# Optimization experiments

Hardware: AMD Instinct MI355X
Metric: run time of the kernel (lower is better)

The kernel has to match this reference:

```python
import jax, jax.numpy as jnp
import numpy as np

R = 16
ALPHA = 32
SCALING = ALPHA / R  # 2.0


def setup_inputs() -> dict:
    key = jax.random.key(0)
    k_x, k_w, k_b, k_a, k_lb, k_o = jax.random.split(key, 6)
    in_f, out_f = 4096, 4096
    x = jax.random.normal(k_x, (4, 4096, in_f), dtype=jnp.float32)
    base_kernel = jax.random.normal(k_w, (in_f, out_f), dtype=jnp.float32) * 0.02
    base_bias = jax.random.normal(k_b, (out_f,), dtype=jnp.float32) * 0.02
    lora_A = jax.random.normal(k_a, (R, R), dtype=jnp.float32)
    lora_B = jax.random.normal(k_lb, (R, R), dtype=jnp.float32) * 0.02
    O = jax.random.normal(k_o, (in_f // R, out_f // R), dtype=jnp.float32)
    return {"x": x, "base_kernel": base_kernel, "base_bias": base_bias,
            "lora_A": lora_A, "lora_B": lora_B, "O": O}


def reference(x, base_kernel, base_bias, lora_A, lora_B, O) -> jnp.ndarray:
    in_f, out_f = base_kernel.shape
    # base path: x @ W + b
    base_out = jnp.dot(x, base_kernel) + base_bias
    # LoKr path: kron(A @ B, O) materialized as in the original module
    w_left = jnp.dot(lora_A, lora_B)                 # (r, r)
    lokr_update = jnp.kron(w_left, O)                # (r*in_factor, r*out_factor)
    lokr_update = lokr_update[:in_f, :out_f]
    lokr_out = jnp.dot(x, lokr_update)
    return base_out + lokr_out * SCALING
```

## Files before the change

### kernel.cpp

```cpp
#include <hip/hip_runtime.h>
#include <stdint.h>
#include <stddef.h>


#define M_TOT 16384
#define K_TOT 4096
#define N_TOT 4096
#define SCALING 2.0f
#define NT (K_TOT / 64)

typedef __attribute__((ext_vector_type(8))) short bf16x8;
typedef __attribute__((ext_vector_type(4))) float floatx4;

__device__ __forceinline__ unsigned short f32_to_bf16(float f) {
  union { float f; unsigned int u; } v; v.f = f;
  unsigned int r = 0x7fffu + ((v.u >> 16) & 1u);
  return (unsigned short)((v.u + r) >> 16);
}

__device__ __forceinline__ void async_copy16(const void* gsrc, void* ldst) {
  __builtin_amdgcn_global_load_lds(
      (const __attribute__((address_space(1))) void*)(uintptr_t)gsrc,
      (__attribute__((address_space(3))) void*)(uintptr_t)ldst,
      16, 0, 0);
}

__global__ void wleft_kernel(const float* __restrict__ A, const float* __restrict__ B,
                             float* __restrict__ wl) {
  int i = threadIdx.x >> 4, j = threadIdx.x & 15;
  float s = 0.f;
#pragma unroll
  for (int k = 0; k < 16; ++k) s += A[i * 16 + k] * B[k * 16 + j];
  wl[threadIdx.x] = s * SCALING;
}

__global__ void prep_w_kernel(const float* __restrict__ base, const float* __restrict__ O,
                              const float* __restrict__ wl, unsigned short* __restrict__ Wt) {
  __shared__ float tile[32][33];
  int n0 = blockIdx.x * 32, k0 = blockIdx.y * 32;
  int tx = threadIdx.x, ty = threadIdx.y;
#pragma unroll
  for (int r = 0; r < 32; r += 8) {
    int k = k0 + ty + r, n = n0 + tx;
    float v = base[(size_t)k * N_TOT + n]
            + wl[((k >> 8) << 4) + (n >> 8)] * O[((size_t)(k & 255) << 8) + (n & 255)];
    tile[ty + r][tx] = v;
  }
  __syncthreads();
#pragma unroll
  for (int r = 0; r < 32; r += 8) {
    int n = n0 + ty + r, k = k0 + tx;
    Wt[(size_t)n * K_TOT + k] = f32_to_bf16(tile[tx][ty + r]);
  }
}

__global__ void cvt_x_kernel(const float* __restrict__ x, unsigned short* __restrict__ xb) {
  size_t i = ((size_t)blockIdx.x * blockDim.x + threadIdx.x) * 8;
  float4 a = *(const float4*)(x + i);
  float4 b = *(const float4*)(x + i + 4);
  union { bf16x8 v; unsigned short h[8]; } u;
  u.h[0] = f32_to_bf16(a.x); u.h[1] = f32_to_bf16(a.y);
  u.h[2] = f32_to_bf16(a.z); u.h[3] = f32_to_bf16(a.w);
  u.h[4] = f32_to_bf16(b.x); u.h[5] = f32_to_bf16(b.y);
  u.h[6] = f32_to_bf16(b.z); u.h[7] = f32_to_bf16(b.w);
  *(bf16x8*)(xb + i) = u.v;
}

__global__ __launch_bounds__(512, 2) void gemm256_kernel(
    const unsigned short* __restrict__ Xb, const unsigned short* __restrict__ Wt,
    const float* __restrict__ bias, float* __restrict__ out) {
  __shared__ __align__(16) unsigned short lds[65536];

  const int tid = threadIdx.x;
  const int wave = tid >> 6, lane = tid & 63;
  const int quad = lane >> 4, lm = lane & 15;
  const int wm = wave >> 2, wn = wave & 3;

  const int wg = blockIdx.x;
  const int swz = (wg & 7) * (1024 / 8) + (wg >> 3);
  const int m0 = (swz >> 4) * 256;
  const int n0 = (swz & 15) * 256;

  const int sch = (tid & 7) ^ ((tid >> 3) & 7);
  const int rowoff = 2 * (tid >> 3) + (sch >> 2);
  const int koff = (sch & 3) * 8;
  const unsigned short* srcA = Xb + (size_t)(m0 + rowoff) * K_TOT + koff;
  const unsigned short* srcB = Wt + (size_t)(n0 + rowoff) * K_TOT + koff;

  const int pch = (((lm & 1) << 2) | quad) ^ (lm >> 1);
  const int aoff = wm * 4096 + (lm >> 1) * 64 + pch * 8;
  const int boff = wn * 2048 + (lm >> 1) * 64 + pch * 8;

  floatx4 acc[8][4];
#pragma unroll
  for (int i = 0; i < 8; ++i)
#pragma unroll
    for (int j = 0; j < 4; ++j) acc[i][j] = (floatx4){0.f, 0.f, 0.f, 0.f};

#define STAGE(tt, ss) do {                                                        \
    unsigned short* la = lds + ((((tt) & 1) * 2 + (ss)) * 8192) + tid * 8;        \
    size_t kk = (size_t)(tt) * 64 + (ss) * 32;                                    \
    async_copy16(srcA + kk, la);                                                  \
    async_copy16(srcA + kk + (size_t)128 * K_TOT, la + 4096);                     \
    async_copy16(srcB + kk, la + 32768);                                          \
    async_copy16(srcB + kk + (size_t)128 * K_TOT, la + 32768 + 4096);             \
  } while (0)

#define COMPUTE(tt, ss) do {                                                      \
    const unsigned short* Ab = lds + ((((tt) & 1) * 2 + (ss)) * 8192) + aoff;     \
    const unsigned short* Bb = lds + 32768 + ((((tt) & 1) * 2 + (ss)) * 8192) + boff; \
    bf16x8 af[8], bfr[4];                                                         \
    _Pragma("unroll") for (int i = 0; i < 8; ++i)                                 \
      af[i] = *(const bf16x8*)(Ab + i * 512);                                     \
    _Pragma("unroll") for (int j = 0; j < 4; ++j)                                 \
      bfr[j] = *(const bf16x8*)(Bb + j * 512);                                    \
    __builtin_amdgcn_s_setprio(1);                                                \
    _Pragma("unroll") for (int i = 0; i < 8; ++i)                                 \
      _Pragma("unroll") for (int j = 0; j < 4; ++j)                               \
        acc[i][j] = __builtin_amdgcn_mfma_f32_16x16x32_bf16(af[i], bfr[j], acc[i][j], 0, 0, 0); \
    __builtin_amdgcn_s_setprio(0);                                                \
  } while (0)

#define WAITBAR(n) do {                                                          \
    asm volatile("s_waitcnt vmcnt(" #n ")" ::: "memory");                        \
    __builtin_amdgcn_s_barrier();                                                \
    asm volatile("" ::: "memory");                                               \
  } while (0)

  STAGE(0, 0);
  STAGE(0, 1);
  STAGE(1, 0);
  WAITBAR(8);

  for (int t = 0; t < NT - 2; ++t) {
    STAGE(t + 1, 1);
    COMPUTE(t, 0);
    WAITBAR(8);
    STAGE(t + 2, 0);
    COMPUTE(t, 1);
    WAITBAR(8);
  }
  STAGE(NT - 1, 1);
  COMPUTE(NT - 2, 0);
  WAITBAR(8);
  COMPUTE(NT - 2, 1);
  WAITBAR(4);
  COMPUTE(NT - 1, 0);
  WAITBAR(0);
  COMPUTE(NT - 1, 1);

#undef STAGE
#undef COMPUTE
#undef WAITBAR

#pragma unroll
  for (int j = 0; j < 4; ++j) {
    int col = n0 + wn * 64 + j * 16 + lm;
    float bv = bias[col];
#pragma unroll
    for (int i = 0; i < 8; ++i) {
      int row = m0 + wm * 128 + i * 16 + quad * 4;
#pragma unroll
      for (int r = 0; r < 4; ++r)
        out[(size_t)(row + r) * N_TOT + col] = acc[i][j][r] + bv;
    }
  }
}

extern "C" void kernel_launch(void* const* d_in, const int* in_sizes, int n_in,
                              void* d_out, int out_size, void* d_ws, size_t ws_size,
                              hipStream_t stream) {
  const float* x    = (const float*)d_in[0];
  const float* base = (const float*)d_in[1];
  const float* bias = (const float*)d_in[2];
  const float* lA   = (const float*)d_in[3];
  const float* lB   = (const float*)d_in[4];
  const float* O    = (const float*)d_in[5];
  float* out = (float*)d_out;

  char* ws = (char*)d_ws;
  unsigned short* Xb = (unsigned short*)ws;
  unsigned short* Wt = (unsigned short*)(ws + (size_t)M_TOT * K_TOT * 2);
  float* wl = (float*)(ws + (size_t)M_TOT * K_TOT * 2 + (size_t)N_TOT * K_TOT * 2);

  wleft_kernel<<<1, 256, 0, stream>>>(lA, lB, wl);
  prep_w_kernel<<<dim3(N_TOT / 32, K_TOT / 32), dim3(32, 8), 0, stream>>>(base, O, wl, Wt);
  cvt_x_kernel<<<((size_t)M_TOT * K_TOT) / 8 / 256, 256, 0, stream>>>(x, Xb);
  gemm256_kernel<<<dim3(1024), 512, 0, stream>>>(Xb, Wt, bias, out);
}
```

Baseline: 959.1 us.

## Interleave GEMM main loop into half-tile phases and vectorize weight prep

The GEMM main loop now runs in four phases per K-tile. Each phase loads half the A fragments from LDS, issues a smaller async stage of A or B, then runs 16 MFMAs, so the two barriers per phase are spread through the loop. This is meant to overlap LDS reads, global-to-LDS copies and MFMA work more finely, at the cost of more barriers per tile. The weight-prep kernel switches to 64x64 tiles with float4 loads, a single hoisted Kronecker scale per block, and 16-byte bf16 stores, which cuts memory transactions.

Measured after the change: 961.9 us. About the same (+0.3%).

```diff
diff --git a/kernel.cpp b/kernel.cpp
--- a/kernel.cpp
+++ b/kernel.cpp
@@ -11,6 +11,7 @@
 
 typedef __attribute__((ext_vector_type(8))) short bf16x8;
 typedef __attribute__((ext_vector_type(4))) float floatx4;
+typedef __attribute__((ext_vector_type(4))) unsigned int uint4v;
 
 __device__ __forceinline__ unsigned short f32_to_bf16(float f) {
   union { float f; unsigned int u; } v; v.f = f;
@@ -36,21 +37,31 @@
 
 __global__ void prep_w_kernel(const float* __restrict__ base, const float* __restrict__ O,
                               const float* __restrict__ wl, unsigned short* __restrict__ Wt) {
-  __shared__ float tile[32][33];
-  int n0 = blockIdx.x * 32, k0 = blockIdx.y * 32;
-  int tx = threadIdx.x, ty = threadIdx.y;
-#pragma unroll
-  for (int r = 0; r < 32; r += 8) {
-    int k = k0 + ty + r, n = n0 + tx;
-    float v = base[(size_t)k * N_TOT + n]
-            + wl[((k >> 8) << 4) + (n >> 8)] * O[((size_t)(k & 255) << 8) + (n & 255)];
-    tile[ty + r][tx] = v;
+  __shared__ float tile[64][65];
+  const int tid = threadIdx.x;
+  const int n0 = blockIdx.x * 64, k0 = blockIdx.y * 64;
+  const float wlv = wl[((k0 >> 8) << 4) + (n0 >> 8)];
+  const float* Obase = O + ((size_t)(k0 & 255) << 8) + (n0 & 255);
+#pragma unroll
+  for (int rep = 0; rep < 4; ++rep) {
+    int idx = rep * 256 + tid;
+    int row = idx >> 4, c4 = (idx & 15) * 4;
+    float4 b4 = *(const float4*)(base + (size_t)(k0 + row) * N_TOT + n0 + c4);
+    float4 o4 = *(const float4*)(Obase + (size_t)row * 256 + c4);
+    tile[row][c4 + 0] = b4.x + wlv * o4.x;
+    tile[row][c4 + 1] = b4.y + wlv * o4.y;
+    tile[row][c4 + 2] = b4.z + wlv * o4.z;
+    tile[row][c4 + 3] = b4.w + wlv * o4.w;
   }
   __syncthreads();
 #pragma unroll
-  for (int r = 0; r < 32; r += 8) {
-    int n = n0 + ty + r, k = k0 + tx;
-    Wt[(size_t)n * K_TOT + k] = f32_to_bf16(tile[tx][ty + r]);
+  for (int rep = 0; rep < 2; ++rep) {
+    int idx = rep * 256 + tid;
+    int n = idx >> 3, kc = (idx & 7) * 8;
+    union { uint4v v; unsigned short h[8]; } u;
+#pragma unroll
+    for (int j = 0; j < 8; ++j) u.h[j] = f32_to_bf16(tile[kc + j][n]);
+    *(uint4v*)(Wt + (size_t)(n0 + n) * K_TOT + k0 + kc) = u.v;
   }
 }
 
@@ -97,61 +108,112 @@
 #pragma unroll
     for (int j = 0; j < 4; ++j) acc[i][j] = (floatx4){0.f, 0.f, 0.f, 0.f};
 
-#define STAGE(tt, ss) do {                                                        \
-    unsigned short* la = lds + ((((tt) & 1) * 2 + (ss)) * 8192) + tid * 8;        \
-    size_t kk = (size_t)(tt) * 64 + (ss) * 32;                                    \
-    async_copy16(srcA + kk, la);                                                  \
-    async_copy16(srcA + kk + (size_t)128 * K_TOT, la + 4096);                     \
-    async_copy16(srcB + kk, la + 32768);                                          \
-    async_copy16(srcB + kk + (size_t)128 * K_TOT, la + 32768 + 4096);             \
-  } while (0)
-
-#define COMPUTE(tt, ss) do {                                                      \
-    const unsigned short* Ab = lds + ((((tt) & 1) * 2 + (ss)) * 8192) + aoff;     \
+  bf16x8 af[4], bf[4];
+
+#define STAGE_A(tt, ss) do {                                                     \
+    unsigned short* la = lds + ((((tt) & 1) * 2 + (ss)) * 8192) + tid * 8;       \
+    size_t kk = (size_t)(tt) * 64 + (ss) * 32;                                   \
+    async_copy16(srcA + kk, la);                                                 \
+    async_copy16(srcA + kk + (size_t)128 * K_TOT, la + 4096);                    \
+  } while (0)
+
+#define STAGE_B(tt, ss) do {                                                     \
+    unsigned short* la = lds + 32768 + ((((tt) & 1) * 2 + (ss)) * 8192) + tid * 8; \
+    size_t kk = (size_t)(tt) * 64 + (ss) * 32;                                   \
+    async_copy16(srcB + kk, la);                                                 \
+    async_copy16(srcB + kk + (size_t)128 * K_TOT, la + 4096);                    \
+  } while (0)
+
+#define LOADB(tt, ss) do {                                                       \
     const unsigned short* Bb = lds + 32768 + ((((tt) & 1) * 2 + (ss)) * 8192) + boff; \
-    bf16x8 af[8], bfr[4];                                                         \
-    _Pragma("unroll") for (int i = 0; i < 8; ++i)                                 \
-      af[i] = *(const bf16x8*)(Ab + i * 512);                                     \
-    _Pragma("unroll") for (int j = 0; j < 4; ++j)                                 \
-      bfr[j] = *(const bf16x8*)(Bb + j * 512);                                    \
-    __builtin_amdgcn_s_setprio(1);                                                \
-    _Pragma("unroll") for (int i = 0; i < 8; ++i)                                 \
-      _Pragma("unroll") for (int j = 0; j < 4; ++j)                               \
-        acc[i][j] = __builtin_amdgcn_mfma_f32_16x16x32_bf16(af[i], bfr[j], acc[i][j], 0, 0, 0); \
-    __builtin_amdgcn_s_setprio(0);                                                \
-  } while (0)
-
-#define WAITBAR(n) do {                                                          \
+    _Pragma("unroll") for (int j = 0; j < 4; ++j)                                \
+      bf[j] = *(const bf16x8*)(Bb + j * 512);                                    \
+  } while (0)
+
+#define LOADA(tt, ss, h) do {                                                    \
+    const unsigned short* Ab = lds + ((((tt) & 1) * 2 + (ss)) * 8192) + aoff;    \
+    _Pragma("unroll") for (int i = 0; i < 4; ++i)                                \
+      af[i] = *(const bf16x8*)(Ab + ((h) * 4 + i) * 512);                        \
+  } while (0)
+
+#define MFMA16(h) do {                                                           \
+    __builtin_amdgcn_s_setprio(1);                                               \
+    _Pragma("unroll") for (int i = 0; i < 4; ++i)                                \
+      _Pragma("unroll") for (int j = 0; j < 4; ++j)                              \
+        acc[(h) * 4 + i][j] =                                                    \
+            __builtin_amdgcn_mfma_f32_16x16x32_bf16(af[i], bf[j], acc[(h) * 4 + i][j], 0, 0, 0); \
+    __builtin_amdgcn_s_setprio(0);                                               \
+  } while (0)
+
+#define SYNC1(n) do {                                                            \
     asm volatile("s_waitcnt vmcnt(" #n ")" ::: "memory");                        \
     __builtin_amdgcn_s_barrier();                                                \
+    asm volatile("s_waitcnt lgkmcnt(0)" ::: "memory");                           \
+  } while (0)
+
+#define BAR2() do {                                                              \
+    __builtin_amdgcn_s_barrier();                                                \
     asm volatile("" ::: "memory");                                               \
   } while (0)
 
-  STAGE(0, 0);
-  STAGE(0, 1);
-  STAGE(1, 0);
-  WAITBAR(8);
-
-  for (int t = 0; t < NT - 2; ++t) {
-    STAGE(t + 1, 1);
-    COMPUTE(t, 0);
-    WAITBAR(8);
-    STAGE(t + 2, 0);
-    COMPUTE(t, 1);
-    WAITBAR(8);
-  }
-  STAGE(NT - 1, 1);
-  COMPUTE(NT - 2, 0);
-  WAITBAR(8);
-  COMPUTE(NT - 2, 1);
-  WAITBAR(4);
-  COMPUTE(NT - 1, 0);
-  WAITBAR(0);
-  COMPUTE(NT - 1, 1);
-
-#undef STAGE
-#undef COMPUTE
-#undef WAITBAR
+  STAGE_A(0, 0);
+  STAGE_B(0, 0);
+  STAGE_A(0, 1);
+  STAGE_B(0, 1);
+  asm volatile("s_waitcnt vmcnt(4)" ::: "memory");
+  __builtin_amdgcn_s_barrier();
+  asm volatile("" ::: "memory");
+
+  for (int t = 0; t < NT - 1; ++t) {
+    LOADB(t, 0); LOADA(t, 0, 0);
+    STAGE_A(t + 1, 0);
+    SYNC1(4);
+    MFMA16(0);
+    BAR2();
+    LOADA(t, 0, 1);
+    STAGE_B(t + 1, 0);
+    SYNC1(4);
+    MFMA16(1);
+    BAR2();
+    LOADB(t, 1); LOADA(t, 1, 0);
+    STAGE_A(t + 1, 1);
+    SYNC1(4);
+    MFMA16(0);
+    BAR2();
+    LOADA(t, 1, 1);
+    STAGE_B(t + 1, 1);
+    SYNC1(4);
+    MFMA16(1);
+    BAR2();
+  }
+
+  {
+    const int t = NT - 1;
+    LOADB(t, 0); LOADA(t, 0, 0);
+    SYNC1(2);
+    MFMA16(0);
+    BAR2();
+    LOADA(t, 0, 1);
+    SYNC1(0);
+    MFMA16(1);
+    BAR2();
+    LOADB(t, 1); LOADA(t, 1, 0);
+    __builtin_amdgcn_s_barrier();
+    asm volatile("s_waitcnt lgkmcnt(0)" ::: "memory");
+    MFMA16(0);
+    BAR2();
+    LOADA(t, 1, 1);
+    asm volatile("s_waitcnt lgkmcnt(0)" ::: "memory");
+    MFMA16(1);
+  }
+
+#undef STAGE_A
+#undef STAGE_B
+#undef LOADB
+#undef LOADA
+#undef MFMA16
+#undef SYNC1
+#undef BAR2
 
 #pragma unroll
   for (int j = 0; j < 4; ++j) {
@@ -184,7 +246,7 @@
   float* wl = (float*)(ws + (size_t)M_TOT * K_TOT * 2 + (size_t)N_TOT * K_TOT * 2);
 
   wleft_kernel<<<1, 256, 0, stream>>>(lA, lB, wl);
-  prep_w_kernel<<<dim3(N_TOT / 32, K_TOT / 32), dim3(32, 8), 0, stream>>>(base, O, wl, Wt);
+  prep_w_kernel<<<dim3(N_TOT / 64, K_TOT / 64), 256, 0, stream>>>(base, O, wl, Wt);
   cvt_x_kernel<<<((size_t)M_TOT * K_TOT) / 8 / 256, 256, 0, stream>>>(x, Xb);
   gemm256_kernel<<<dim3(1024), 512, 0, stream>>>(Xb, Wt, bias, out);
 }
```
